# Performance work log

Hardware: AMD Instinct MI355X
Metric: run time of the kernel (lower is better)

The kernel has to match this reference:

```python
import jax, jax.numpy as jnp
import numpy as np

B, T, K = 256, 512, 128


def setup_inputs() -> dict:
    key = jax.random.key(0)
    k1, k2, k3, k4 = jax.random.split(key, 4)
    emissions = jax.random.normal(k1, (B, T, K), jnp.float32)
    tag_ids = jax.random.randint(k2, (B, T), 0, K, dtype=jnp.int32)
    lengths = jnp.maximum(jax.random.randint(k3, (B,), 0, T + 1, dtype=jnp.int32), 1)
    # learned CRF transition matrix (transition_weight * learning_rate_multiplier)
    transitions = jax.random.normal(k4, (K, K), jnp.float32) * 0.1
    return {"emissions": emissions, "tag_ids": tag_ids, "lengths": lengths,
            "transitions": transitions}


def _log_norm(emissions, transitions, lengths):
    # forward algorithm (log-sum-exp semiring scan over time)
    t = emissions.shape[1]
    alpha0 = emissions[:, 0]  # [B,K]
    valid = jnp.arange(1, t)[:, None] < lengths[None, :]  # [T-1,B]

    def step(alpha, inp):
        emit_t, v = inp  # [B,K], [B]
        new = jax.nn.logsumexp(alpha[:, :, None] + transitions[None], axis=1) + emit_t
        return jnp.where(v[:, None], new, alpha), None

    alpha, _ = jax.lax.scan(step, alpha0, (jnp.swapaxes(emissions[:, 1:], 0, 1), valid))
    return jax.nn.logsumexp(alpha, axis=-1)  # [B]


def _sequence_score(emissions, transitions, tag_ids, lengths):
    t = emissions.shape[1]
    mask = (jnp.arange(t)[None, :] < lengths[:, None]).astype(emissions.dtype)  # [B,T]
    unary = jnp.take_along_axis(emissions, tag_ids[..., None], axis=-1)[..., 0]  # [B,T]
    unary_score = jnp.sum(unary * mask, axis=1)
    pair = transitions[tag_ids[:, :-1], tag_ids[:, 1:]]  # [B,T-1]
    binary_score = jnp.sum(pair * mask[:, 1:], axis=1)  # prefix mask: t+1 valid => t valid
    return unary_score + binary_score


def _viterbi_decode(emissions, transitions, lengths):
    t = emissions.shape[1]
    k = emissions.shape[2]
    v0 = emissions[:, 0]  # [B,K]
    valid = jnp.arange(1, t)[:, None] < lengths[None, :]  # [T-1,B]
    identity_bp = jnp.arange(k, dtype=jnp.int32)[None, :]  # pass-through for padding

    def fwd(v, inp):
        emit_t, va = inp
        scores = v[:, :, None] + transitions[None]  # [B,K,K]
        bp = jnp.argmax(scores, axis=1).astype(jnp.int32)  # [B,K]
        new = jnp.max(scores, axis=1) + emit_t
        v_new = jnp.where(va[:, None], new, v)
        bp = jnp.where(va[:, None], bp, identity_bp)
        return v_new, bp

    v_final, bps = jax.lax.scan(fwd, v0, (jnp.swapaxes(emissions[:, 1:], 0, 1), valid))
    last_tag = jnp.argmax(v_final, axis=-1).astype(jnp.int32)  # [B]

    def back(tag, bp_t):
        prev = jnp.take_along_axis(bp_t, tag[:, None], axis=1)[:, 0]
        return prev, tag  # emit tag_{t+1}, carry tag_t

    first_tag, tags_rest = jax.lax.scan(back, last_tag, bps, reverse=True)
    decoded = jnp.concatenate([first_tag[None], tags_rest], axis=0)  # [T,B]
    return jnp.swapaxes(decoded, 0, 1)  # [B,T]


def reference(emissions, tag_ids, lengths, transitions):
    log_likelihood = _sequence_score(emissions, transitions, tag_ids, lengths) \
        - _log_norm(emissions, transitions, lengths)
    loss = -jnp.mean(log_likelihood)
    decoded = _viterbi_decode(emissions, transitions, lengths)
    mask = (jnp.arange(emissions.shape[1])[None, :] < lengths[:, None]).astype(jnp.int32)
    is_equal = (tag_ids == decoded).astype(jnp.int32)
    tag_accuracy = jnp.sum(is_equal * mask) / jnp.sum(mask)
    return loss, decoded, tag_accuracy
```

## Files before the change

kernel.cpp:

```cpp
#include <hip/hip_runtime.h>

#define T_ 512
#define K_ 128
#define B_ 256
#define PADH 68


__global__ __launch_bounds__(256, 2) void crf_main(
    const float* __restrict__ emissions,
    const int* __restrict__ tag_ids,
    const int* __restrict__ lengths,
    const float* __restrict__ transitions,
    float* __restrict__ out,
    float* __restrict__ ws_ll,
    int* __restrict__ ws_cnt)
{
    const int bid = blockIdx.x;
    const int tid = threadIdx.x;

    if (bid < B_) {
        __shared__ __align__(16) float eaBuf[2][2 * PADH];
        __shared__ __align__(16) float wmax[4];
        __shared__ float redLDS[4];

        const int b   = bid;
        const int len = lengths[b];
        const float* emB = emissions + (size_t)b * T_ * K_;
        const int*  tagB = tag_ids + b * T_;

        {
            float s = 0.f;
            #pragma unroll
            for (int h = 0; h < 2; ++h) {
                int t = tid + h * 256;
                if (t < len) {
                    int tg = tagB[t];
                    float v = emB[t * K_ + tg];
                    if (t >= 1) v += transitions[tagB[t - 1] * K_ + tg];
                    s += v;
                }
            }
            #pragma unroll
            for (int m = 1; m < 64; m <<= 1) s += __shfl_xor(s, m);
            if ((tid & 63) == 0) redLDS[tid >> 6] = s;
        }

        const int j = tid >> 1;
        const int c = tid & 1;
        const int wiA = (j >> 6) * PADH + (j & 63);

        float tbl[64];
        #pragma unroll
        for (int k = 0; k < 64; ++k)
            tbl[k] = __expf(transitions[(c * 64 + k) * K_ + j]);

        {
            float e0 = emB[j];
            if (c == 0) eaBuf[0][wiA] = __expf(e0);
            float wm = e0;
            #pragma unroll
            for (int m = 1; m < 64; m <<= 1) wm = fmaxf(wm, __shfl_xor(wm, m));
            if ((tid & 63) == 0) wmax[tid >> 6] = wm;
        }
        __syncthreads();

        int cur = 0;
        float Sr = 0.f;
        float emN = emB[K_ + j];

        for (int t = 1; t < len; ++t) {
            float emC = emN;
            int tn = (t + 1 < T_) ? (t + 1) : t;
            emN = emB[tn * K_ + j];

            float Sw;
            if (((t - 1) & 3) == 0) {
                float4 wv = *(const float4*)&wmax[0];
                Sw = fmaxf(fmaxf(wv.x, wv.y), fmaxf(wv.z, wv.w));
            } else Sw = Sr;

            const float* ea = &eaBuf[cur][c * PADH];
            float a0 = 0.f, a1 = 0.f, a2 = 0.f, a3 = 0.f;
            #pragma unroll
            for (int k = 0; k < 16; ++k) {
                float4 e4 = *(const float4*)(ea + 4 * k);
                a0 = fmaf(e4.x, tbl[4 * k + 0], a0);
                a1 = fmaf(e4.y, tbl[4 * k + 1], a1);
                a2 = fmaf(e4.z, tbl[4 * k + 2], a2);
                a3 = fmaf(e4.w, tbl[4 * k + 3], a3);
            }
            float dot = (a0 + a1) + (a2 + a3);
            dot += __shfl_xor(dot, 1);

            float an = __logf(dot) + Sr + emC;
            if (c == 0) eaBuf[cur ^ 1][wiA] = __expf(an - Sw);
            Sr = Sw;

            if (((t - 1) & 3) == 3) {
                float wm = an;
                #pragma unroll
                for (int m = 1; m < 64; m <<= 1) wm = fmaxf(wm, __shfl_xor(wm, m));
                if ((tid & 63) == 0) wmax[tid >> 6] = wm;
            }
            cur ^= 1;
            __syncthreads();
        }

        float logZv = 0.f;
        if (tid < 64) {
            float s = eaBuf[cur][tid] + eaBuf[cur][PADH + tid];
            #pragma unroll
            for (int m = 1; m < 64; m <<= 1) s += __shfl_xor(s, m);
            logZv = Sr + __logf(s);
        }
        if (tid == 0) {
            float sc = redLDS[0] + redLDS[1] + redLDS[2] + redLDS[3];
            ws_ll[b] = sc - logZv;
        }

    } else {
        __shared__ unsigned char bpLDS[T_ * K_];
        __shared__ __align__(16) float vaBuf[2][2 * PADH];
        __shared__ unsigned char decLDS[T_];
        __shared__ int redILDS[4];
        __shared__ int ltagLDS;

        const int b   = bid - B_;
        const int len = lengths[b];
        const float* emB = emissions + (size_t)b * T_ * K_;
        const int*  tagB = tag_ids + b * T_;

        const int j = tid >> 1;
        const int c = tid & 1;
        const int wiA = (j >> 6) * PADH + (j & 63);

        float tbl[64];
        #pragma unroll
        for (int k = 0; k < 64; ++k)
            tbl[k] = transitions[(c * 64 + k) * K_ + j];

        {
            float e0 = emB[j];
            if (c == 0) vaBuf[0][wiA] = e0;
        }
        __syncthreads();

        int cur = 0;
        float emN = emB[K_ + j];

        for (int t = 1; t < len; ++t) {
            float emC = emN;
            int tn = (t + 1 < T_) ? (t + 1) : t;
            emN = emB[tn * K_ + j];

            const float* va = &vaBuf[cur][c * PADH];
            float v0[16];
            int   g0[16];
            #pragma unroll
            for (int k = 0; k < 16; ++k) {
                float4 v4 = *(const float4*)(va + 4 * k);
                float s0 = v4.x + tbl[4 * k + 0];
                float s1 = v4.y + tbl[4 * k + 1];
                float s2 = v4.z + tbl[4 * k + 2];
                float s3 = v4.w + tbl[4 * k + 3];
                float mA; int aA;
                if (s1 > s0) { mA = s1; aA = 4 * k + 1; } else { mA = s0; aA = 4 * k + 0; }
                float mC; int aC;
                if (s3 > s2) { mC = s3; aC = 4 * k + 3; } else { mC = s2; aC = 4 * k + 2; }
                if (mC > mA) { v0[k] = mC; g0[k] = aC; } else { v0[k] = mA; g0[k] = aA; }
            }
            #pragma unroll
            for (int st = 1; st < 16; st <<= 1) {
                #pragma unroll
                for (int k = 0; k < 16; k += 2 * st) {
                    if (v0[k + st] > v0[k]) { v0[k] = v0[k + st]; g0[k] = g0[k + st]; }
                }
            }
            float mB = v0[0];
            int  arg = g0[0] + c * 64;

            float om = __shfl_xor(mB, 1);
            int   oa = __shfl_xor(arg, 1);
            float mLow  = c ? om : mB;   int aLow  = c ? oa : arg;
            float mHigh = c ? mB : om;   int aHigh = c ? arg : oa;
            float mF; int aF;
            if (mHigh > mLow) { mF = mHigh; aF = aHigh; } else { mF = mLow; aF = aLow; }
            if (c == 0) {
                vaBuf[cur ^ 1][wiA] = mF + emC;
                bpLDS[t * K_ + j] = (unsigned char)aF;
            }
            cur ^= 1;
            __syncthreads();
        }

        if (tid < 64) {
            int l = tid;
            float m = vaBuf[cur][l]; int a = l;
            float v2 = vaBuf[cur][PADH + l];
            if (v2 > m) { m = v2; a = l + 64; }
            #pragma unroll
            for (int sft = 1; sft < 64; sft <<= 1) {
                float om = __shfl_xor(m, sft);
                int   oa = __shfl_xor(a, sft);
                if (om > m || (om == m && oa < a)) { m = om; a = oa; }
            }
            if (l == 0) ltagLDS = a;
        }
        __syncthreads();

        if (tid == 0) {
            int tg = ltagLDS;
            for (int t = T_ - 1; t >= 1; --t) {
                decLDS[t] = (unsigned char)tg;
                if (t < len) tg = bpLDS[t * K_ + tg];
            }
            decLDS[0] = (unsigned char)tg;
        }
        __syncthreads();

        {
            int good = 0;
            #pragma unroll
            for (int h = 0; h < 2; ++h) {
                int t = tid + h * 256;
                int dv = decLDS[t];
                out[1 + b * T_ + t] = (float)dv;
                good += (t < len && tagB[t] == dv) ? 1 : 0;
            }
            #pragma unroll
            for (int m = 1; m < 64; m <<= 1) good += __shfl_xor(good, m);
            if ((tid & 63) == 0) redILDS[tid >> 6] = good;
        }
        __syncthreads();

        if (tid == 0)
            ws_cnt[b] = redILDS[0] + redILDS[1] + redILDS[2] + redILDS[3];
    }
}

__global__ void crf_final(const float* __restrict__ ws_ll,
                          const int* __restrict__ ws_cnt,
                          const int* __restrict__ lengths,
                          float* __restrict__ out)
{
    __shared__ float sll[4];
    __shared__ int scnt[4], slen[4];
    int tid = threadIdx.x;
    float ll = ws_ll[tid];
    int   cn = ws_cnt[tid];
    int   L  = lengths[tid];
    #pragma unroll
    for (int m = 1; m < 64; m <<= 1) {
        ll += __shfl_xor(ll, m);
        cn += __shfl_xor(cn, m);
        L  += __shfl_xor(L, m);
    }
    if ((tid & 63) == 0) { sll[tid >> 6] = ll; scnt[tid >> 6] = cn; slen[tid >> 6] = L; }
    __syncthreads();
    if (tid == 0) {
        float llS = sll[0] + sll[1] + sll[2] + sll[3];
        int   cS  = scnt[0] + scnt[1] + scnt[2] + scnt[3];
        int   LS  = slen[0] + slen[1] + slen[2] + slen[3];
        out[0] = -llS / (float)B_;
        out[1 + B_ * T_] = (float)cS / (float)LS;
    }
}

extern "C" void kernel_launch(void* const* d_in, const int* in_sizes, int n_in,
                              void* d_out, int out_size, void* d_ws, size_t ws_size,
                              hipStream_t stream) {
    const float* emissions   = (const float*)d_in[0];
    const int*   tag_ids     = (const int*)d_in[1];
    const int*   lengths     = (const int*)d_in[2];
    const float* transitions = (const float*)d_in[3];
    float* out = (float*)d_out;

    float* ws_ll  = (float*)d_ws;
    int*   ws_cnt = (int*)((char*)d_ws + B_ * sizeof(float));

    crf_main<<<2 * B_, 256, 0, stream>>>(emissions, tag_ids, lengths, transitions,
                                         out, ws_ll, ws_cnt);
    crf_final<<<1, B_, 0, stream>>>(ws_ll, ws_cnt, lengths, out);
}
```

Baseline: 563.9 us.

## Split Viterbi into single-wave max scan, parallel backpointer pass, and backtrack kernel

The forward and Viterbi recurrences now run in one 64-lane wave per sequence, so there are no block barriers. Each lane handles two tags and keeps the full transition columns in registers. The Viterbi scan only computes max scores and stores every step's scores to a global buffer. A separate kernel then recomputes argmax backpointers in parallel over four time chunks per sequence, and a third kernel backtracks and computes scores. This takes the argmax and barrier work off the serial critical path, at the cost of extra global traffic, 256-entry per-thread register tables that may spill, and more launches.

```diff
diff --git a/kernel.cpp b/kernel.cpp
--- a/kernel.cpp
+++ b/kernel.cpp
@@ -3,238 +3,269 @@
 #define T_ 512
 #define K_ 128
 #define B_ 256
-#define PADH 68
-
-
-__global__ __launch_bounds__(256, 2) void crf_main(
+
+__device__ float         g_v[B_][T_][K_];
+__device__ unsigned char g_bp[B_][T_][K_];
+
+
+__global__ __launch_bounds__(64, 1) void crf_serial(
+    const float* __restrict__ emissions,
+    const int* __restrict__ lengths,
+    const float* __restrict__ transitions,
+    float* __restrict__ ws_logZ)
+{
+    const int bid = blockIdx.x;
+    const int l   = threadIdx.x;
+
+    if (bid < B_) {
+        __shared__ __align__(16) float ea[K_];
+        const int b   = bid;
+        const int len = lengths[b];
+        const float* emB = emissions + (size_t)b * T_ * K_;
+
+        float tA[128], tB[128];
+        #pragma unroll
+        for (int i = 0; i < 128; ++i) {
+            tA[i] = __expf(transitions[i * K_ + l]);
+            tB[i] = __expf(transitions[i * K_ + l + 64]);
+        }
+
+        float e0 = emB[l], e1 = emB[l + 64];
+        ea[l]      = __expf(e0);
+        ea[l + 64] = __expf(e1);
+        float wm = fmaxf(e0, e1);
+        #pragma unroll
+        for (int m = 1; m < 64; m <<= 1) wm = fmaxf(wm, __shfl_xor(wm, m));
+        float Wm = wm;
+        float Sr = 0.f;
+
+        float eN0 = emB[K_ + l], eN1 = emB[K_ + l + 64];
+
+        for (int t = 1; t < len; ++t) {
+            float ec0 = eN0, ec1 = eN1;
+            int tn = (t + 1 < T_) ? (t + 1) : t;
+            eN0 = emB[tn * K_ + l]; eN1 = emB[tn * K_ + l + 64];
+
+            float Sw = (((t - 1) & 3) == 0) ? Wm : Sr;
+
+            float a0=0.f,a1=0.f,a2=0.f,a3=0.f, c0=0.f,c1=0.f,c2=0.f,c3=0.f;
+            #pragma unroll
+            for (int m = 0; m < 32; ++m) {
+                float4 q = *(const float4*)&ea[4 * m];
+                a0 = fmaf(q.x, tA[4*m+0], a0);
+                a1 = fmaf(q.y, tA[4*m+1], a1);
+                a2 = fmaf(q.z, tA[4*m+2], a2);
+                a3 = fmaf(q.w, tA[4*m+3], a3);
+                c0 = fmaf(q.x, tB[4*m+0], c0);
+                c1 = fmaf(q.y, tB[4*m+1], c1);
+                c2 = fmaf(q.z, tB[4*m+2], c2);
+                c3 = fmaf(q.w, tB[4*m+3], c3);
+            }
+            float d0 = (a0 + a1) + (a2 + a3);
+            float d1 = (c0 + c1) + (c2 + c3);
+            float an0 = __logf(d0) + Sr + ec0;
+            float an1 = __logf(d1) + Sr + ec1;
+            ea[l]      = __expf(an0 - Sw);
+            ea[l + 64] = __expf(an1 - Sw);
+            Sr = Sw;
+            if (((t - 1) & 3) == 3) {
+                float w = fmaxf(an0, an1);
+                #pragma unroll
+                for (int m = 1; m < 64; m <<= 1) w = fmaxf(w, __shfl_xor(w, m));
+                Wm = w;
+            }
+        }
+        float s = ea[l] + ea[l + 64];
+        #pragma unroll
+        for (int m = 1; m < 64; m <<= 1) s += __shfl_xor(s, m);
+        if (l == 0) ws_logZ[b] = Sr + __logf(s);
+
+    } else {
+        __shared__ __align__(16) float va[K_];
+        const int b   = bid - B_;
+        const int len = lengths[b];
+        const float* emB = emissions + (size_t)b * T_ * K_;
+
+        float tA[128], tB[128];
+        #pragma unroll
+        for (int i = 0; i < 128; ++i) {
+            tA[i] = transitions[i * K_ + l];
+            tB[i] = transitions[i * K_ + l + 64];
+        }
+
+        float v0 = emB[l], v1 = emB[l + 64];
+        va[l] = v0; va[l + 64] = v1;
+        g_v[b][0][l] = v0; g_v[b][0][l + 64] = v1;
+
+        float eN0 = emB[K_ + l], eN1 = emB[K_ + l + 64];
+
+        for (int t = 1; t < len; ++t) {
+            float ec0 = eN0, ec1 = eN1;
+            int tn = (t + 1 < T_) ? (t + 1) : t;
+            eN0 = emB[tn * K_ + l]; eN1 = emB[tn * K_ + l + 64];
+
+            float r0 = -3.4028235e38f, r1 = r0, r2 = r0, r3 = r0;
+            #pragma unroll
+            for (int m = 0; m < 32; ++m) {
+                float4 q = *(const float4*)&va[4 * m];
+                r0 = fmaxf(r0, fmaxf(q.x + tA[4*m+0], q.y + tA[4*m+1]));
+                r1 = fmaxf(r1, fmaxf(q.z + tA[4*m+2], q.w + tA[4*m+3]));
+                r2 = fmaxf(r2, fmaxf(q.x + tB[4*m+0], q.y + tB[4*m+1]));
+                r3 = fmaxf(r3, fmaxf(q.z + tB[4*m+2], q.w + tB[4*m+3]));
+            }
+            float vn0 = fmaxf(r0, r1) + ec0;
+            float vn1 = fmaxf(r2, r3) + ec1;
+            va[l] = vn0; va[l + 64] = vn1;
+            g_v[b][t][l] = vn0; g_v[b][t][l + 64] = vn1;
+        }
+    }
+}
+
+__global__ __launch_bounds__(256, 2) void crf_bp(
+    const int* __restrict__ lengths,
+    const float* __restrict__ transitions)
+{
+    const int b     = blockIdx.x >> 2;
+    const int chunk = blockIdx.x & 3;
+    const int len   = lengths[b];
+    const int tid   = threadIdx.x;
+    const int j = tid >> 1;
+    const int c = tid & 1;
+
+    int t0 = 1 + chunk * 128;
+    int t1 = t0 + 128; if (t1 > len) t1 = len;
+    if (t0 >= t1) return;
+
+    float tbl[64];
+    #pragma unroll
+    for (int k = 0; k < 64; ++k)
+        tbl[k] = transitions[(c * 64 + k) * K_ + j];
+
+    for (int t = t0; t < t1; ++t) {
+        const float* vp = &g_v[b][t - 1][c * 64];
+        float v0[16]; int gg[16];
+        #pragma unroll
+        for (int k = 0; k < 16; ++k) {
+            float4 v4 = *(const float4*)(vp + 4 * k);
+            float s0 = v4.x + tbl[4*k+0];
+            float s1 = v4.y + tbl[4*k+1];
+            float s2 = v4.z + tbl[4*k+2];
+            float s3 = v4.w + tbl[4*k+3];
+            float mA; int aA;
+            if (s1 > s0) { mA = s1; aA = 4*k+1; } else { mA = s0; aA = 4*k+0; }
+            float mC; int aC;
+            if (s3 > s2) { mC = s3; aC = 4*k+3; } else { mC = s2; aC = 4*k+2; }
+            if (mC > mA) { v0[k] = mC; gg[k] = aC; } else { v0[k] = mA; gg[k] = aA; }
+        }
+        #pragma unroll
+        for (int st = 1; st < 16; st <<= 1) {
+            #pragma unroll
+            for (int k = 0; k < 16; k += 2 * st) {
+                if (v0[k+st] > v0[k]) { v0[k] = v0[k+st]; gg[k] = gg[k+st]; }
+            }
+        }
+        float mB = v0[0];
+        int  arg = gg[0] + c * 64;
+        float om = __shfl_xor(mB, 1);
+        int   oa = __shfl_xor(arg, 1);
+        float mLow  = c ? om : mB;   int aLow  = c ? oa : arg;
+        float mHigh = c ? mB : om;   int aHigh = c ? arg : oa;
+        int aF = (mHigh > mLow) ? aHigh : aLow;
+        if (c == 0) g_bp[b][t][j] = (unsigned char)aF;
+    }
+}
+
+__global__ __launch_bounds__(256, 2) void crf_back(
     const float* __restrict__ emissions,
     const int* __restrict__ tag_ids,
     const int* __restrict__ lengths,
     const float* __restrict__ transitions,
     float* __restrict__ out,
     float* __restrict__ ws_ll,
-    int* __restrict__ ws_cnt)
+    int* __restrict__ ws_cnt,
+    const float* __restrict__ ws_logZ)
 {
-    const int bid = blockIdx.x;
+    __shared__ __align__(16) unsigned char bpL[T_ * K_];
+    __shared__ unsigned char decL[T_];
+    __shared__ float redS[4];
+    __shared__ int  redI[4];
+    __shared__ int  ltag;
+
+    const int b   = blockIdx.x;
     const int tid = threadIdx.x;
-
-    if (bid < B_) {
-        __shared__ __align__(16) float eaBuf[2][2 * PADH];
-        __shared__ __align__(16) float wmax[4];
-        __shared__ float redLDS[4];
-
-        const int b   = bid;
-        const int len = lengths[b];
-        const float* emB = emissions + (size_t)b * T_ * K_;
-        const int*  tagB = tag_ids + b * T_;
-
-        {
-            float s = 0.f;
-            #pragma unroll
-            for (int h = 0; h < 2; ++h) {
-                int t = tid + h * 256;
-                if (t < len) {
-                    int tg = tagB[t];
-                    float v = emB[t * K_ + tg];
-                    if (t >= 1) v += transitions[tagB[t - 1] * K_ + tg];
-                    s += v;
-                }
-            }
-            #pragma unroll
-            for (int m = 1; m < 64; m <<= 1) s += __shfl_xor(s, m);
-            if ((tid & 63) == 0) redLDS[tid >> 6] = s;
-        }
-
-        const int j = tid >> 1;
-        const int c = tid & 1;
-        const int wiA = (j >> 6) * PADH + (j & 63);
-
-        float tbl[64];
-        #pragma unroll
-        for (int k = 0; k < 64; ++k)
-            tbl[k] = __expf(transitions[(c * 64 + k) * K_ + j]);
-
-        {
-            float e0 = emB[j];
-            if (c == 0) eaBuf[0][wiA] = __expf(e0);
-            float wm = e0;
-            #pragma unroll
-            for (int m = 1; m < 64; m <<= 1) wm = fmaxf(wm, __shfl_xor(wm, m));
-            if ((tid & 63) == 0) wmax[tid >> 6] = wm;
-        }
-        __syncthreads();
-
-        int cur = 0;
-        float Sr = 0.f;
-        float emN = emB[K_ + j];
-
-        for (int t = 1; t < len; ++t) {
-            float emC = emN;
-            int tn = (t + 1 < T_) ? (t + 1) : t;
-            emN = emB[tn * K_ + j];
-
-            float Sw;
-            if (((t - 1) & 3) == 0) {
-                float4 wv = *(const float4*)&wmax[0];
-                Sw = fmaxf(fmaxf(wv.x, wv.y), fmaxf(wv.z, wv.w));
-            } else Sw = Sr;
-
-            const float* ea = &eaBuf[cur][c * PADH];
-            float a0 = 0.f, a1 = 0.f, a2 = 0.f, a3 = 0.f;
-            #pragma unroll
-            for (int k = 0; k < 16; ++k) {
-                float4 e4 = *(const float4*)(ea + 4 * k);
-                a0 = fmaf(e4.x, tbl[4 * k + 0], a0);
-                a1 = fmaf(e4.y, tbl[4 * k + 1], a1);
-                a2 = fmaf(e4.z, tbl[4 * k + 2], a2);
-                a3 = fmaf(e4.w, tbl[4 * k + 3], a3);
-            }
-            float dot = (a0 + a1) + (a2 + a3);
-            dot += __shfl_xor(dot, 1);
-
-            float an = __logf(dot) + Sr + emC;
-            if (c == 0) eaBuf[cur ^ 1][wiA] = __expf(an - Sw);
-            Sr = Sw;
-
-            if (((t - 1) & 3) == 3) {
-                float wm = an;
-                #pragma unroll
-                for (int m = 1; m < 64; m <<= 1) wm = fmaxf(wm, __shfl_xor(wm, m));
-                if ((tid & 63) == 0) wmax[tid >> 6] = wm;
-            }
-            cur ^= 1;
-            __syncthreads();
-        }
-
-        float logZv = 0.f;
-        if (tid < 64) {
-            float s = eaBuf[cur][tid] + eaBuf[cur][PADH + tid];
-            #pragma unroll
-            for (int m = 1; m < 64; m <<= 1) s += __shfl_xor(s, m);
-            logZv = Sr + __logf(s);
-        }
-        if (tid == 0) {
-            float sc = redLDS[0] + redLDS[1] + redLDS[2] + redLDS[3];
-            ws_ll[b] = sc - logZv;
-        }
-
-    } else {
-        __shared__ unsigned char bpLDS[T_ * K_];
-        __shared__ __align__(16) float vaBuf[2][2 * PADH];
-        __shared__ unsigned char decLDS[T_];
-        __shared__ int redILDS[4];
-        __shared__ int ltagLDS;
-
-        const int b   = bid - B_;
-        const int len = lengths[b];
-        const float* emB = emissions + (size_t)b * T_ * K_;
-        const int*  tagB = tag_ids + b * T_;
-
-        const int j = tid >> 1;
-        const int c = tid & 1;
-        const int wiA = (j >> 6) * PADH + (j & 63);
-
-        float tbl[64];
-        #pragma unroll
-        for (int k = 0; k < 64; ++k)
-            tbl[k] = transitions[(c * 64 + k) * K_ + j];
-
-        {
-            float e0 = emB[j];
-            if (c == 0) vaBuf[0][wiA] = e0;
-        }
-        __syncthreads();
-
-        int cur = 0;
-        float emN = emB[K_ + j];
-
-        for (int t = 1; t < len; ++t) {
-            float emC = emN;
-            int tn = (t + 1 < T_) ? (t + 1) : t;
-            emN = emB[tn * K_ + j];
-
-            const float* va = &vaBuf[cur][c * PADH];
-            float v0[16];
-            int   g0[16];
-            #pragma unroll
-            for (int k = 0; k < 16; ++k) {
-                float4 v4 = *(const float4*)(va + 4 * k);
-                float s0 = v4.x + tbl[4 * k + 0];
-                float s1 = v4.y + tbl[4 * k + 1];
-                float s2 = v4.z + tbl[4 * k + 2];
-                float s3 = v4.w + tbl[4 * k + 3];
-                float mA; int aA;
-                if (s1 > s0) { mA = s1; aA = 4 * k + 1; } else { mA = s0; aA = 4 * k + 0; }
-                float mC; int aC;
-                if (s3 > s2) { mC = s3; aC = 4 * k + 3; } else { mC = s2; aC = 4 * k + 2; }
-                if (mC > mA) { v0[k] = mC; g0[k] = aC; } else { v0[k] = mA; g0[k] = aA; }
-            }
-            #pragma unroll
-            for (int st = 1; st < 16; st <<= 1) {
-                #pragma unroll
-                for (int k = 0; k < 16; k += 2 * st) {
-                    if (v0[k + st] > v0[k]) { v0[k] = v0[k + st]; g0[k] = g0[k + st]; }
-                }
-            }
-            float mB = v0[0];
-            int  arg = g0[0] + c * 64;
-
-            float om = __shfl_xor(mB, 1);
-            int   oa = __shfl_xor(arg, 1);
-            float mLow  = c ? om : mB;   int aLow  = c ? oa : arg;
-            float mHigh = c ? mB : om;   int aHigh = c ? arg : oa;
-            float mF; int aF;
-            if (mHigh > mLow) { mF = mHigh; aF = aHigh; } else { mF = mLow; aF = aLow; }
-            if (c == 0) {
-                vaBuf[cur ^ 1][wiA] = mF + emC;
-                bpLDS[t * K_ + j] = (unsigned char)aF;
-            }
-            cur ^= 1;
-            __syncthreads();
-        }
-
-        if (tid < 64) {
-            int l = tid;
-            float m = vaBuf[cur][l]; int a = l;
-            float v2 = vaBuf[cur][PADH + l];
-            if (v2 > m) { m = v2; a = l + 64; }
-            #pragma unroll
-            for (int sft = 1; sft < 64; sft <<= 1) {
-                float om = __shfl_xor(m, sft);
-                int   oa = __shfl_xor(a, sft);
-                if (om > m || (om == m && oa < a)) { m = om; a = oa; }
-            }
-            if (l == 0) ltagLDS = a;
-        }
-        __syncthreads();
-
-        if (tid == 0) {
-            int tg = ltagLDS;
-            for (int t = T_ - 1; t >= 1; --t) {
-                decLDS[t] = (unsigned char)tg;
-                if (t < len) tg = bpLDS[t * K_ + tg];
-            }
-            decLDS[0] = (unsigned char)tg;
-        }
-        __syncthreads();
-
-        {
-            int good = 0;
-            #pragma unroll
-            for (int h = 0; h < 2; ++h) {
-                int t = tid + h * 256;
-                int dv = decLDS[t];
-                out[1 + b * T_ + t] = (float)dv;
-                good += (t < len && tagB[t] == dv) ? 1 : 0;
-            }
-            #pragma unroll
-            for (int m = 1; m < 64; m <<= 1) good += __shfl_xor(good, m);
-            if ((tid & 63) == 0) redILDS[tid >> 6] = good;
-        }
-        __syncthreads();
-
-        if (tid == 0)
-            ws_cnt[b] = redILDS[0] + redILDS[1] + redILDS[2] + redILDS[3];
+    const int len = lengths[b];
+    const float* emB = emissions + (size_t)b * T_ * K_;
+    const int*  tagB = tag_ids + b * T_;
+
+    {
+        const uint4* src = (const uint4*)&g_bp[b][0][0];
+        uint4* dst = (uint4*)&bpL[0];
+        #pragma unroll
+        for (int it = 0; it < 16; ++it)
+            dst[it * 256 + tid] = src[it * 256 + tid];
+    }
+
+    {
+        float s = 0.f;
+        #pragma unroll
+        for (int h = 0; h < 2; ++h) {
+            int t = tid + h * 256;
+            if (t < len) {
+                int tg = tagB[t];
+                float v = emB[t * K_ + tg];
+                if (t >= 1) v += transitions[tagB[t - 1] * K_ + tg];
+                s += v;
+            }
+        }
+        #pragma unroll
+        for (int m = 1; m < 64; m <<= 1) s += __shfl_xor(s, m);
+        if ((tid & 63) == 0) redS[tid >> 6] = s;
+    }
+
+    if (tid < 64) {
+        const float* vf = &g_v[b][len - 1][0];
+        int l = tid;
+        float m = vf[l]; int a = l;
+        float v2 = vf[l + 64];
+        if (v2 > m) { m = v2; a = l + 64; }
+        #pragma unroll
+        for (int sft = 1; sft < 64; sft <<= 1) {
+            float om = __shfl_xor(m, sft);
+            int   oa = __shfl_xor(a, sft);
+            if (om > m || (om == m && oa < a)) { m = om; a = oa; }
+        }
+        if (l == 0) ltag = a;
+    }
+    __syncthreads();
+
+    if (tid == 0) {
+        int tg = ltag;
+        for (int t = T_ - 1; t >= 1; --t) {
+            decL[t] = (unsigned char)tg;
+            if (t < len) tg = bpL[t * K_ + tg];
+        }
+        decL[0] = (unsigned char)tg;
+    }
+    __syncthreads();
+
+    {
+        int good = 0;
+        #pragma unroll
+        for (int h = 0; h < 2; ++h) {
+            int t = tid + h * 256;
+            int dv = decL[t];
+            out[1 + b * T_ + t] = (float)dv;
+            good += (t < len && tagB[t] == dv) ? 1 : 0;
+        }
+        #pragma unroll
+        for (int m = 1; m < 64; m <<= 1) good += __shfl_xor(good, m);
+        if ((tid & 63) == 0) redI[tid >> 6] = good;
+    }
+    __syncthreads();
+
+    if (tid == 0) {
+        ws_cnt[b] = redI[0] + redI[1] + redI[2] + redI[3];
+        ws_ll[b]  = (redS[0] + redS[1] + redS[2] + redS[3]) - ws_logZ[b];
     }
 }
 
@@ -275,10 +306,13 @@
     const float* transitions = (const float*)d_in[3];
     float* out = (float*)d_out;
 
-    float* ws_ll  = (float*)d_ws;
-    int*   ws_cnt = (int*)((char*)d_ws + B_ * sizeof(float));
-
-    crf_main<<<2 * B_, 256, 0, stream>>>(emissions, tag_ids, lengths, transitions,
-                                         out, ws_ll, ws_cnt);
+    float* ws_ll   = (float*)d_ws;
+    int*   ws_cnt  = (int*)((char*)d_ws + B_ * sizeof(float));
+    float* ws_logZ = (float*)((char*)d_ws + 2 * B_ * sizeof(float));
+
+    crf_serial<<<2 * B_, 64, 0, stream>>>(emissions, lengths, transitions, ws_logZ);
+    crf_bp<<<4 * B_, 256, 0, stream>>>(lengths, transitions);
+    crf_back<<<B_, 256, 0, stream>>>(emissions, tag_ids, lengths, transitions,
+                                     out, ws_ll, ws_cnt, ws_logZ);
     crf_final<<<1, B_, 0, stream>>>(ws_ll, ws_cnt, lengths, out);
 }
```

Measured after the change: 1.495 ms. 165% more time.
